# Optimization experiments

Measured on AMD Instinct MI355X. Metric: run time of the kernel, lower is better.

The kernel has to match this reference:

```python
import jax, jax.numpy as jnp
import numpy as np

B, C, L = 32, 512, 16          # batch, clauses per CNF, max literals per clause
D, H, P = 256, 1024, 16        # clause_hidden_dim, hidden_size, prefix_tokens
NH, NL = 8, 4                  # adapter_heads, adapter_layers
MAXV = 512                     # max_variables


def _ln(x, w, b, eps=1e-5):
    m = jnp.mean(x, axis=-1, keepdims=True)
    v = jnp.mean(jnp.square(x - m), axis=-1, keepdims=True)
    return (x - m) * jax.lax.rsqrt(v + eps) * w + b


def _mha(q, k, v, w_in, b_in, w_out, b_out, nh):
    E = q.shape[-1]
    dh = E // nh
    wq, wk, wv = jnp.split(w_in, 3, axis=0)
    bq, bk, bv = jnp.split(b_in, 3, axis=0)

    def heads(x, w, b):
        y = x @ w.T + b
        return y.reshape(x.shape[0], x.shape[1], nh, dh).transpose(0, 2, 1, 3)

    qh, kh, vh = heads(q, wq, bq), heads(k, wk, bk), heads(v, wv, bv)
    att = jax.nn.softmax(jnp.einsum('bhqd,bhkd->bhqk', qh, kh) * (1.0 / np.sqrt(dh)), axis=-1)
    o = jnp.einsum('bhqk,bhkd->bhqd', att, vh).transpose(0, 2, 1, 3).reshape(q.shape[0], q.shape[1], E)
    return o @ w_out.T + b_out


def setup_inputs() -> dict:
    key = jax.random.key(0)
    ks = jax.random.split(key, 16)
    s = 0.02
    var_idx = jax.random.randint(ks[0], (B, C, L), 0, MAXV + 1)
    sign_idx = jax.random.randint(ks[1], (B, C, L), 1, 3)   # 1=positive literal, 2=negative
    lens = jax.random.randint(ks[2], (B, C), 1, L + 1)      # ragged clause lengths >= 1
    lit_mask = jnp.arange(L)[None, None, :] < lens[..., None]
    inp = dict(var_idx=var_idx, sign_idx=sign_idx, lit_mask=lit_mask)
    inp['var_emb'] = jax.random.normal(ks[3], (MAXV + 1, D)) * s
    inp['sign_emb'] = jax.random.normal(ks[4], (3, D)) * s
    inp['litpos_emb'] = jax.random.normal(ks[5], (L, D)) * s
    inp['clausepos_emb'] = jax.random.normal(ks[6], (C, D)) * s
    inp['enc_in_w'] = jax.random.normal(ks[7], (NL, 3 * D, D)) * s
    inp['enc_in_b'] = jnp.zeros((NL, 3 * D))
    inp['enc_out_w'] = jax.random.normal(ks[8], (NL, D, D)) * s
    inp['enc_out_b'] = jnp.zeros((NL, D))
    inp['enc_ff1_w'] = jax.random.normal(ks[9], (NL, 4 * D, D)) * s
    inp['enc_ff1_b'] = jnp.zeros((NL, 4 * D))
    inp['enc_ff2_w'] = jax.random.normal(ks[10], (NL, D, 4 * D)) * s
    inp['enc_ff2_b'] = jnp.zeros((NL, D))
    inp['enc_n1_w'] = jnp.ones((NL, D))
    inp['enc_n1_b'] = jnp.zeros((NL, D))
    inp['enc_n2_w'] = jnp.ones((NL, D))
    inp['enc_n2_b'] = jnp.zeros((NL, D))
    inp['th_ln_w'] = jnp.ones((D,))
    inp['th_ln_b'] = jnp.zeros((D,))
    inp['th_w'] = jax.random.normal(ks[11], (H, D)) * s
    inp['th_b'] = jnp.zeros((H,))
    inp['pq'] = jax.random.normal(ks[12], (P, H))
    inp['pa_in_w'] = jax.random.normal(ks[13], (3 * H, H)) * s
    inp['pa_in_b'] = jnp.zeros((3 * H,))
    inp['pa_out_w'] = jax.random.normal(ks[14], (H, H)) * s
    inp['pa_out_b'] = jnp.zeros((H,))
    inp['pn_w'] = jnp.ones((H,))
    inp['pn_b'] = jnp.zeros((H,))
    return inp


def reference(var_idx, sign_idx, lit_mask, var_emb, sign_emb, litpos_emb, clausepos_emb,
              enc_in_w, enc_in_b, enc_out_w, enc_out_b, enc_ff1_w, enc_ff1_b,
              enc_ff2_w, enc_ff2_b, enc_n1_w, enc_n1_b, enc_n2_w, enc_n2_b,
              th_ln_w, th_ln_b, th_w, th_b, pq, pa_in_w, pa_in_b, pa_out_w, pa_out_b,
              pn_w, pn_b):
    # literal states [B,C,L,D]: four embedding gathers fused into one expression
    lit = (var_emb[var_idx] + sign_emb[sign_idx]
           + litpos_emb[None, None, :, :] + clausepos_emb[None, :, None, :])
    m = lit_mask[..., None].astype(lit.dtype)
    x = jnp.sum(lit * m, axis=2) / jnp.sum(m, axis=2)   # masked mean-pool -> [B,C,D]
    for i in range(NL):  # PyTorch post-norm TransformerEncoderLayer, gelu (exact)
        a = _mha(x, x, x, enc_in_w[i], enc_in_b[i], enc_out_w[i], enc_out_b[i], NH)
        x = _ln(x + a, enc_n1_w[i], enc_n1_b[i])
        f = jax.nn.gelu(x @ enc_ff1_w[i].T + enc_ff1_b[i], approximate=False) @ enc_ff2_w[i].T + enc_ff2_b[i]
        x = _ln(x + f, enc_n2_w[i], enc_n2_b[i])
    ch = _ln(x, th_ln_w, th_ln_b) @ th_w.T + th_b       # to_hidden -> [B,C,H]
    q = jnp.broadcast_to(pq[None], (ch.shape[0], P, H))
    pref = _mha(q, ch, ch, pa_in_w, pa_in_b, pa_out_w, pa_out_b, NH)
    return _ln(pref + q, pn_w, pn_b)                    # [B,P,H]
```

## Files before the change

kernel.cpp:

```cpp
#include <hip/hip_runtime.h>
#include <hip/hip_bf16.h>

typedef unsigned short u16;
typedef unsigned int u32;
typedef __attribute__((ext_vector_type(8))) short short8;
typedef __attribute__((ext_vector_type(4))) float floatx4;

#define BB 32
#define CC 512
#define LL 16
#define DD 256
#define HH 1024
#define PP 16
#define NLAY 4

__device__ __forceinline__ float bf2f(u16 u) {
  u32 x = ((u32)u) << 16; float f; __builtin_memcpy(&f, &x, 4); return f;
}
__device__ __forceinline__ u16 f2bf(float f) {
  __hip_bfloat16 h = __float2bfloat16(f);
  u16 r; __builtin_memcpy(&r, &h, 2); return r;
}
__device__ __forceinline__ void gload_lds16(const u16* g, u16* l) {
  __builtin_amdgcn_global_load_lds(
      (const __attribute__((address_space(1))) void*)g,
      (__attribute__((address_space(3))) void*)l, 16, 0, 0);
}

__global__ __launch_bounds__(256) void cvt_kernel(
    const float* __restrict__ s0, const float* __restrict__ s1,
    const float* __restrict__ s2, const float* __restrict__ s3,
    const float* __restrict__ s4, const float* __restrict__ s5,
    const float* __restrict__ s6, const float* __restrict__ s7,
    const float* __restrict__ s8, const float* __restrict__ s9,
    const float* __restrict__ s10, const float* __restrict__ s11,
    u16* __restrict__ dst)
{
  const float* srcs[12] = {s0, s1, s2, s3, s4, s5, s6, s7, s8, s9, s10, s11};
  const int pfx[12] = {786432, 1048576, 2097152, 3145728, 3407872, 6553600, 7602176,
                       7618560, 7749888, 7750656, 7754752, 7885824};
  int e = (blockIdx.x * 256 + threadIdx.x) * 4;
  int seg = 0;
  while (e >= pfx[seg]) seg++;
  int start = seg ? pfx[seg - 1] : 0;
  float4 f = *(const float4*)(srcs[seg] + (e - start));
  u16 o[4] = {f2bf(f.x), f2bf(f.y), f2bf(f.z), f2bf(f.w)};
  *(uint2*)(dst + e) = *(const uint2*)o;
}

__global__ __launch_bounds__(256) void thwT_kernel(
    const float* __restrict__ thw, u16* __restrict__ out)
{
  __shared__ float tile[32][33];
  int bx = blockIdx.x & 7, by = blockIdx.x >> 3;
  int tx = threadIdx.x & 31, ty = threadIdx.x >> 5;
  #pragma unroll
  for (int i = 0; i < 4; ++i) {
    int h = by * 32 + ty + i * 8, d = bx * 32 + tx;
    tile[ty + i * 8][tx] = thw[h * 256 + d];
  }
  __syncthreads();
  #pragma unroll
  for (int i = 0; i < 4; ++i) {
    int d = bx * 32 + ty + i * 8, h = by * 32 + tx;
    out[d * 1024 + h] = f2bf(tile[tx][ty + i * 8]);
  }
}

__global__ __launch_bounds__(256) void bT_kernel(
    const u16* __restrict__ in, u16* __restrict__ out)
{
  __shared__ u16 tile[32][33];
  int bx = blockIdx.x & 7, by = blockIdx.x >> 3;
  int tx = threadIdx.x & 31, ty = threadIdx.x >> 5;
  #pragma unroll
  for (int i = 0; i < 4; ++i) {
    int hd = by * 32 + ty + i * 8, c = bx * 32 + tx;
    tile[ty + i * 8][tx] = in[hd * 256 + c];
  }
  __syncthreads();
  #pragma unroll
  for (int i = 0; i < 4; ++i) {
    int c = bx * 32 + ty + i * 8, hd = by * 32 + tx;
    out[c * 1024 + hd] = tile[tx][ty + i * 8];
  }
}

__global__ __launch_bounds__(256) void qc_kernel(
    const u16* __restrict__ qh, const u16* __restrict__ wckT, u16* __restrict__ qcg)
{
  int h = blockIdx.x;
  int t = threadIdx.x, lane = t & 63, w = t >> 6;
  int mrow = lane & 15, quad = lane >> 4;
  const floatx4 zf = (floatx4){0.f, 0.f, 0.f, 0.f};
  floatx4 acc[4] = {zf, zf, zf, zf};
  #pragma unroll
  for (int kk = 0; kk < 4; ++kk) {
    short8 af = *(const short8*)(qh + (size_t)mrow * 1024 + h * 128 + kk * 32 + quad * 8);
    #pragma unroll
    for (int ct = 0; ct < 4; ++ct) {
      int c = w * 64 + ct * 16 + mrow;
      short8 bf = *(const short8*)(wckT + (size_t)c * 1024 + h * 128 + kk * 32 + quad * 8);
      acc[ct] = __builtin_amdgcn_mfma_f32_16x16x32_bf16(af, bf, acc[ct], 0, 0, 0);
    }
  }
  #pragma unroll
  for (int ct = 0; ct < 4; ++ct)
    #pragma unroll
    for (int r = 0; r < 4; ++r)
      qcg[((size_t)h * 16 + quad * 4 + r) * 256 + w * 64 + ct * 16 + mrow] = f2bf(acc[ct][r]);
}

__global__ __launch_bounds__(256) void biasfold_kernel(
    const u16* __restrict__ Wkv, const float* __restrict__ thb,
    const float* __restrict__ paib, float* __restrict__ out)
{
  int wv = threadIdx.x >> 6, lane = threadIdx.x & 63;
  int n = blockIdx.x * 4 + wv;
  const u16* wr = Wkv + (size_t)n * 1024;
  float s = 0.f;
  #pragma unroll
  for (int i = 0; i < 16; ++i) {
    int h = i * 64 + lane;
    s += bf2f(wr[h]) * thb[h];
  }
  #pragma unroll
  for (int off = 32; off; off >>= 1) s += __shfl_xor(s, off);
  if (!lane) out[n] = s + paib[1024 + n];
}

__global__ __launch_bounds__(256) void redk_kernel(
    const float* __restrict__ part, const float* __restrict__ bias,
    const float* __restrict__ res, float* __restrict__ outf, u16* __restrict__ outb,
    int N, int nz, int total, int flags)
{
  int idx = (blockIdx.x * 256 + threadIdx.x) * 4;
  if (idx >= total) return;
  float4 a = *(const float4*)(part + idx);
  for (int z = 1; z < nz; ++z) {
    float4 b = *(const float4*)(part + (size_t)z * total + idx);
    a.x += b.x; a.y += b.y; a.z += b.z; a.w += b.w;
  }
  int row = idx / N, col = idx - row * N;
  float v4[4] = {a.x, a.y, a.z, a.w};
  #pragma unroll
  for (int i = 0; i < 4; ++i) {
    if (bias) v4[i] += bias[col + i];
    if (res) v4[i] += res[(size_t)((flags & 4) ? (row & 15) : row) * N + col + i];
  }
  if (outf) {
    *(float4*)(outf + idx) = *(const float4*)v4;
  } else {
    u16 o[4] = {f2bf(v4[0]), f2bf(v4[1]), f2bf(v4[2]), f2bf(v4[3])};
    *(uint2*)(outb + idx) = *(const uint2*)o;
  }
}

__global__ __launch_bounds__(256) void embed_kernel(
    const int* __restrict__ vi, const int* __restrict__ si, const int* __restrict__ mk,
    const u16* __restrict__ veb, const u16* __restrict__ seb,
    const u16* __restrict__ lpeb, const u16* __restrict__ cpeb,
    u16* __restrict__ xb)
{
  int t = threadIdx.x;
  int bc = blockIdx.x * 2 + (t >> 7);
  int c = bc & (CC - 1);
  int dl = (t & 127) * 2;
  int base = bc * LL;
  float a0 = 0.f, a1 = 0.f; int cnt = 0;
  #pragma unroll
  for (int l = 0; l < LL; ++l) {
    if (mk[base + l]) {
      int v = vi[base + l], s = si[base + l];
      u32 vv = *(const u32*)&veb[v * DD + dl];
      u32 sv = *(const u32*)&seb[s * DD + dl];
      u32 lv = *(const u32*)&lpeb[l * DD + dl];
      a0 += bf2f((u16)vv) + bf2f((u16)sv) + bf2f((u16)lv);
      a1 += bf2f((u16)(vv >> 16)) + bf2f((u16)(sv >> 16)) + bf2f((u16)(lv >> 16));
      cnt++;
    }
  }
  u32 cv = *(const u32*)&cpeb[c * DD + dl];
  float inv = 1.f / (float)cnt;
  u32 pk = (u32)f2bf(a0 * inv + bf2f((u16)cv)) | ((u32)f2bf(a1 * inv + bf2f((u16)(cv >> 16))) << 16);
  *(u32*)&xb[(size_t)bc * DD + dl] = pk;
}

template<int NC, bool GELU, bool LN, bool DLN>
__global__ __launch_bounds__(256) void gwide_kernel(
    const u16* __restrict__ A, const u16* __restrict__ W, const float* __restrict__ bias,
    const u16* __restrict__ resb, const float* __restrict__ gam, const float* __restrict__ bet,
    const float* __restrict__ gam2, const float* __restrict__ bet2,
    u16* __restrict__ out, int N, int K)
{
  constexpr int NT = NC / 32;
  constexpr int NT4 = NC / 64;
  __shared__ __align__(16) u16 As[32 * 64];
  __shared__ __align__(16) u16 Ws[NC * 64];
  __shared__ float sred[32][4][2];
  __shared__ float sred2[32][4][2];
  int t = threadIdx.x, lane = t & 63, w = t >> 6;
  int mrow = lane & 15, quad = lane >> 4;
  int bn0 = blockIdx.x * NC, bm0 = blockIdx.y * 32;

  int rA = t >> 3, gcA = (t & 7) ^ (rA & 7);
  const u16* gAp = A + (size_t)(bm0 + rA) * K + gcA * 8;
  u16* lAp = As + (w * 64) * 8;
  const u16* gW0 = W + (size_t)(bn0 + rA) * K + gcA * 8;
  u16* lW0 = Ws + (w * 64) * 8;

  floatx4 acc[2][NT4];
  #pragma unroll
  for (int mi = 0; mi < 2; ++mi)
    #pragma unroll
    for (int nt = 0; nt < NT4; ++nt) acc[mi][nt] = (floatx4){0.f, 0.f, 0.f, 0.f};

  for (int k0 = 0; k0 < K; k0 += 64) {
    __syncthreads();
    gload_lds16(gAp, lAp); gAp += 64;
    #pragma unroll
    for (int i = 0; i < NT; ++i)
      gload_lds16(gW0 + (size_t)i * 32 * K, lW0 + i * 2048);
    gW0 += 64;
    __syncthreads();
    #pragma unroll
    for (int ks = 0; ks < 2; ++ks) {
      int sw = ((ks * 4 + quad) ^ (mrow & 7)) * 8;
      short8 af0 = *(const short8*)&As[mrow * 64 + sw];
      short8 af1 = *(const short8*)&As[(16 + mrow) * 64 + sw];
      #pragma unroll
      for (int nt = 0; nt < NT4; ++nt) {
        int rw = w * (NC / 4) + nt * 16 + mrow;
        short8 bf = *(const short8*)&Ws[rw * 64 + sw];
        acc[0][nt] = __builtin_amdgcn_mfma_f32_16x16x32_bf16(af0, bf, acc[0][nt], 0, 0, 0);
        acc[1][nt] = __builtin_amdgcn_mfma_f32_16x16x32_bf16(af1, bf, acc[1][nt], 0, 0, 0);
      }
    }
  }

  if constexpr (LN) {
    float val[2][NT4][4];
    float bv[NT4];
    #pragma unroll
    for (int nt = 0; nt < NT4; ++nt) bv[nt] = bias[w * 64 + nt * 16 + mrow];
    #pragma unroll
    for (int mi = 0; mi < 2; ++mi) {
      #pragma unroll
      for (int r = 0; r < 4; ++r) {
        int gm = bm0 + mi * 16 + quad * 4 + r;
        float sr = 0.f, s2r = 0.f;
        #pragma unroll
        for (int nt = 0; nt < NT4; ++nt) {
          int gn = w * 64 + nt * 16 + mrow;
          float v = acc[mi][nt][r] + bv[nt] + bf2f(resb[(size_t)gm * 256 + gn]);
          val[mi][nt][r] = v; sr += v; s2r += v * v;
        }
        sr += __shfl_xor(sr, 1); s2r += __shfl_xor(s2r, 1);
        sr += __shfl_xor(sr, 2); s2r += __shfl_xor(s2r, 2);
        sr += __shfl_xor(sr, 4); s2r += __shfl_xor(s2r, 4);
        sr += __shfl_xor(sr, 8); s2r += __shfl_xor(s2r, 8);
        if (mrow == 0) { sred[mi * 16 + quad * 4 + r][w][0] = sr; sred[mi * 16 + quad * 4 + r][w][1] = s2r; }
      }
    }
    __syncthreads();
    #pragma unroll
    for (int mi = 0; mi < 2; ++mi) {
      #pragma unroll
      for (int r = 0; r < 4; ++r) {
        int lrow = mi * 16 + quad * 4 + r;
        float S  = sred[lrow][0][0] + sred[lrow][1][0] + sred[lrow][2][0] + sred[lrow][3][0];
        float S2 = sred[lrow][0][1] + sred[lrow][1][1] + sred[lrow][2][1] + sred[lrow][3][1];
        float mean = S * (1.f / 256.f);
        float var = S2 * (1.f / 256.f) - mean * mean;
        float inv = rsqrtf(var + 1e-5f);
        float sr2 = 0.f, s2r2 = 0.f;
        #pragma unroll
        for (int nt = 0; nt < NT4; ++nt) {
          int gn = w * 64 + nt * 16 + mrow;
          float y = (val[mi][nt][r] - mean) * inv * gam[gn] + bet[gn];
          val[mi][nt][r] = y;
          if constexpr (DLN) { sr2 += y; s2r2 += y * y; }
          else out[(size_t)(bm0 + lrow) * 256 + gn] = f2bf(y);
        }
        if constexpr (DLN) {
          sr2 += __shfl_xor(sr2, 1); s2r2 += __shfl_xor(s2r2, 1);
          sr2 += __shfl_xor(sr2, 2); s2r2 += __shfl_xor(s2r2, 2);
          sr2 += __shfl_xor(sr2, 4); s2r2 += __shfl_xor(s2r2, 4);
          sr2 += __shfl_xor(sr2, 8); s2r2 += __shfl_xor(s2r2, 8);
          if (mrow == 0) { sred2[lrow][w][0] = sr2; sred2[lrow][w][1] = s2r2; }
        }
      }
    }
    if constexpr (DLN) {
      __syncthreads();
      #pragma unroll
      for (int mi = 0; mi < 2; ++mi) {
        #pragma unroll
        for (int r = 0; r < 4; ++r) {
          int lrow = mi * 16 + quad * 4 + r;
          float S  = sred2[lrow][0][0] + sred2[lrow][1][0] + sred2[lrow][2][0] + sred2[lrow][3][0];
          float S2 = sred2[lrow][0][1] + sred2[lrow][1][1] + sred2[lrow][2][1] + sred2[lrow][3][1];
          float mean = S * (1.f / 256.f);
          float var = S2 * (1.f / 256.f) - mean * mean;
          float inv = rsqrtf(var + 1e-5f);
          #pragma unroll
          for (int nt = 0; nt < NT4; ++nt) {
            int gn = w * 64 + nt * 16 + mrow;
            float z = (val[mi][nt][r] - mean) * inv * gam2[gn] + bet2[gn];
            out[(size_t)(bm0 + lrow) * 256 + gn] = f2bf(z);
          }
        }
      }
    }
  } else {
    #pragma unroll
    for (int nt = 0; nt < NT4; ++nt) {
      int gn = bn0 + w * (NC / 4) + nt * 16 + mrow;
      float bv = bias[gn];
      #pragma unroll
      for (int mi = 0; mi < 2; ++mi) {
        #pragma unroll
        for (int r = 0; r < 4; ++r) {
          int gm = bm0 + mi * 16 + quad * 4 + r;
          float v = acc[mi][nt][r] + bv;
          if (GELU) v = 0.5f * v * (1.f + erff(v * 0.70710678118654752f));
          out[(size_t)gm * N + gn] = f2bf(v);
        }
      }
    }
  }
}

__global__ __launch_bounds__(256) void gemm128_kernel(
    const u16* __restrict__ A, const u16* __restrict__ W, const float* __restrict__ bias,
    const float* __restrict__ res, void* __restrict__ out,
    int M, int N, int K, int flags)
{
  __shared__ __align__(16) u16 As[128 * 64];
  __shared__ __align__(16) u16 Bs[128 * 64];
  int t = threadIdx.x;
  int lane = t & 63, w = t >> 6;
  int wm = w & 1, wn = w >> 1;
  int bn0 = blockIdx.x * 128, bm0 = blockIdx.y * 128;
  int mrow = lane & 15, quad = lane >> 4;
  int z = blockIdx.z, NZ = gridDim.z;
  int Kc = K / NZ, kbase = z * Kc;

  const u16* gA[4]; const u16* gB[4];
  u16* lA[4]; u16* lB[4];
  #pragma unroll
  for (int it = 0; it < 4; ++it) {
    int c = w * 256 + it * 64 + lane;
    int r = c >> 3;
    int gc = (c & 7) ^ (r & 7);
    gA[it] = A + (size_t)(bm0 + r) * K + kbase + gc * 8;
    gB[it] = W + (size_t)(bn0 + r) * K + kbase + gc * 8;
    lA[it] = As + (w * 256 + it * 64) * 8;
    lB[it] = Bs + (w * 256 + it * 64) * 8;
  }
  floatx4 acc[4][4];
  #pragma unroll
  for (int i = 0; i < 4; ++i)
    #pragma unroll
    for (int j = 0; j < 4; ++j)
      acc[i][j] = (floatx4){0.f, 0.f, 0.f, 0.f};
  int sw0 = ((0 * 4 + quad) ^ (mrow & 7)) * 8;
  int sw1 = ((1 * 4 + quad) ^ (mrow & 7)) * 8;

  for (int k0 = 0; k0 < Kc; k0 += 64) {
    __syncthreads();
    #pragma unroll
    for (int it = 0; it < 4; ++it) { gload_lds16(gA[it], lA[it]); gA[it] += 64; }
    #pragma unroll
    for (int it = 0; it < 4; ++it) { gload_lds16(gB[it], lB[it]); gB[it] += 64; }
    __syncthreads();
    #pragma unroll
    for (int ks = 0; ks < 2; ++ks) {
      int sw = ks ? sw1 : sw0;
      short8 af[4], bfr[4];
      #pragma unroll
      for (int mi = 0; mi < 4; ++mi)
        af[mi] = *(const short8*)&As[(wm * 64 + mi * 16 + mrow) * 64 + sw];
      #pragma unroll
      for (int nj = 0; nj < 4; ++nj)
        bfr[nj] = *(const short8*)&Bs[(wn * 64 + nj * 16 + mrow) * 64 + sw];
      #pragma unroll
      for (int mi = 0; mi < 4; ++mi)
        #pragma unroll
        for (int nj = 0; nj < 4; ++nj)
          acc[mi][nj] = __builtin_amdgcn_mfma_f32_16x16x32_bf16(af[mi], bfr[nj], acc[mi][nj], 0, 0, 0);
    }
  }
  if (NZ > 1) {
    float* po = (float*)out + (size_t)z * M * N;
    #pragma unroll
    for (int nj = 0; nj < 4; ++nj) {
      int gn = bn0 + wn * 64 + nj * 16 + mrow;
      #pragma unroll
      for (int mi = 0; mi < 4; ++mi)
        #pragma unroll
        for (int r = 0; r < 4; ++r) {
          int gm = bm0 + wm * 64 + mi * 16 + quad * 4 + r;
          po[(size_t)gm * N + gn] = acc[mi][nj][r];
        }
    }
    return;
  }
  bool do_gelu = (flags & 1) != 0, of32 = (flags & 2) != 0;
  #pragma unroll
  for (int nj = 0; nj < 4; ++nj) {
    int gn = bn0 + wn * 64 + nj * 16 + mrow;
    float bv = bias ? bias[gn] : 0.f;
    #pragma unroll
    for (int mi = 0; mi < 4; ++mi) {
      #pragma unroll
      for (int r = 0; r < 4; ++r) {
        int gm = bm0 + wm * 64 + mi * 16 + quad * 4 + r;
        float v = acc[mi][nj][r] + bv;
        if (do_gelu) v = 0.5f * v * (1.f + erff(v * 0.70710678118654752f));
        if (flags & 4) v += res[(size_t)(gm & 15) * N + gn];
        else if (res) v += res[(size_t)gm * N + gn];
        if (of32) ((float*)out)[(size_t)gm * N + gn] = v;
        else      ((u16*)out)[(size_t)gm * N + gn] = f2bf(v);
      }
    }
  }
}

template<int D>
__global__ __launch_bounds__(256) void lnw_kernel(
    const float* __restrict__ in, const float* __restrict__ w, const float* __restrict__ b,
    float* __restrict__ outf, u16* __restrict__ outb)
{
  constexpr int NV = D / 64;
  int lane = threadIdx.x & 63, wv = threadIdx.x >> 6;
  int row = blockIdx.x * 4 + wv;
  const float* xr = in + (size_t)row * D;
  float v[NV];
  float s = 0.f, s2 = 0.f;
  #pragma unroll
  for (int i = 0; i < NV; ++i) {
    v[i] = xr[lane + i * 64];
    s += v[i]; s2 += v[i] * v[i];
  }
  #pragma unroll
  for (int off = 32; off > 0; off >>= 1) { s += __shfl_xor(s, off); s2 += __shfl_xor(s2, off); }
  float mean = s / (float)D;
  float var = s2 / (float)D - mean * mean;
  float inv = rsqrtf(var + 1e-5f);
  #pragma unroll
  for (int i = 0; i < NV; ++i) {
    int col = lane + i * 64;
    float y = (v[i] - mean) * inv * w[col] + b[col];
    size_t o = (size_t)row * D + col;
    if (outf) outf[o] = y;
    if (outb) outb[o] = f2bf(y);
  }
}

__global__ __launch_bounds__(256, 5) void attn_enc6_kernel(
    const u16* __restrict__ qkv, u16* __restrict__ out)
{
  __shared__ __align__(16) u16 Ks[64 * 40];
  __shared__ __align__(16) u16 Vt[32 * 72];
  __shared__ __align__(16) u16 Pl[4 * 32 * 72];
  int F = blockIdx.x;
  int xcd = F & 7, jj = F >> 3;
  int pair = xcd * 32 + (jj >> 2), qt = jj & 3;
  int b = pair >> 3, h = pair & 7;
  int t = threadIdx.x, lane = t & 63, w = t >> 6;
  int mrow = lane & 15, quad = lane >> 4;
  int q0 = qt * 128 + w * 32;
  short8 qf[2];
  #pragma unroll
  for (int mi = 0; mi < 2; ++mi)
    qf[mi] = *(const short8*)(qkv + (size_t)(b * CC + q0 + mi * 16 + mrow) * 768 + h * 32 + quad * 8);
  floatx4 o[2][2];
  #pragma unroll
  for (int mi = 0; mi < 2; ++mi)
    #pragma unroll
    for (int di = 0; di < 2; ++di) o[mi][di] = (floatx4){0.f, 0.f, 0.f, 0.f};
  float lst[2][4] = {{0.f,0.f,0.f,0.f},{0.f,0.f,0.f,0.f}};
  const float sc = 0.17677669529663687f * 1.4426950408889634f;
  const floatx4 zf = (floatx4){0.f, 0.f, 0.f, 0.f};
  for (int jt = 0; jt < 8; ++jt) {
    if (jt) __syncthreads();
    {
      int j = t >> 2, q4 = (t & 3) * 8;
      uint4 kk = *(const uint4*)(qkv + (size_t)(b * CC + jt * 64 + j) * 768 + 256 + h * 32 + q4);
      *(uint4*)&Ks[j * 40 + q4] = kk;
      uint4 vv = *(const uint4*)(qkv + (size_t)(b * CC + jt * 64 + j) * 768 + 512 + h * 32 + q4);
      u16 tmp[8]; *(uint4*)tmp = vv;
      int jp = (j & 15) * 4 + (j >> 4);
      #pragma unroll
      for (int i = 0; i < 8; ++i) Vt[(q4 + i) * 72 + jp] = tmp[i];
    }
    __syncthreads();
    floatx4 s[2][4];
    #pragma unroll
    for (int nj = 0; nj < 4; ++nj) {
      short8 bf = *(const short8*)&Ks[(nj * 16 + mrow) * 40 + quad * 8];
      s[0][nj] = __builtin_amdgcn_mfma_f32_16x16x32_bf16(qf[0], bf, zf, 0, 0, 0);
      s[1][nj] = __builtin_amdgcn_mfma_f32_16x16x32_bf16(qf[1], bf, zf, 0, 0, 0);
    }
    #pragma unroll
    for (int mi = 0; mi < 2; ++mi) {
      #pragma unroll
      for (int r = 0; r < 4; ++r) {
        float ps = 0.f; u16 hv[4];
        #pragma unroll
        for (int nj = 0; nj < 4; ++nj) {
          float p = exp2f(s[mi][nj][r] * sc);
          ps += p; hv[nj] = f2bf(p);
        }
        lst[mi][r] += ps;
        *(uint2*)&Pl[(w * 32 + mi * 16 + quad * 4 + r) * 72 + mrow * 4] = *(uint2*)hv;
      }
    }
    #pragma unroll
    for (int ks = 0; ks < 2; ++ks) {
      short8 a0 = *(const short8*)&Pl[(w * 32 + mrow) * 72 + ks * 32 + quad * 8];
      short8 a1 = *(const short8*)&Pl[(w * 32 + 16 + mrow) * 72 + ks * 32 + quad * 8];
      short8 b0 = *(const short8*)&Vt[mrow * 72 + ks * 32 + quad * 8];
      short8 b1 = *(const short8*)&Vt[(16 + mrow) * 72 + ks * 32 + quad * 8];
      o[0][0] = __builtin_amdgcn_mfma_f32_16x16x32_bf16(a0, b0, o[0][0], 0, 0, 0);
      o[0][1] = __builtin_amdgcn_mfma_f32_16x16x32_bf16(a0, b1, o[0][1], 0, 0, 0);
      o[1][0] = __builtin_amdgcn_mfma_f32_16x16x32_bf16(a1, b0, o[1][0], 0, 0, 0);
      o[1][1] = __builtin_amdgcn_mfma_f32_16x16x32_bf16(a1, b1, o[1][1], 0, 0, 0);
    }
  }
  #pragma unroll
  for (int mi = 0; mi < 2; ++mi) {
    #pragma unroll
    for (int r = 0; r < 4; ++r) {
      float l = lst[mi][r];
      l += __shfl_xor(l, 1); l += __shfl_xor(l, 2);
      l += __shfl_xor(l, 4); l += __shfl_xor(l, 8);
      float inv = 1.f / l;
      int row = b * CC + q0 + mi * 16 + quad * 4 + r;
      #pragma unroll
      for (int di = 0; di < 2; ++di)
        out[(size_t)row * DD + h * 32 + di * 16 + mrow] = f2bf(o[mi][di][r] * inv);
    }
  }
}

__global__ __launch_bounds__(256) void attn_preff_kernel(
    const u16* __restrict__ tln, const u16* __restrict__ wcb,
    const u16* __restrict__ qcg, const float* __restrict__ bkv,
    u16* __restrict__ out)
{
  __shared__ __align__(16) u16 Ajc[64 * 264];
  __shared__ __align__(16) u16 Acj[256 * 72];
  __shared__ __align__(16) u16 Qs[16 * 264];
  __shared__ __align__(16) u16 Ps[16 * 72];
  __shared__ __align__(16) u16 Ts[16 * 264];
  __shared__ float Lred[4][16];
  int b = blockIdx.x, h = blockIdx.y;
  int t = threadIdx.x, lane = t & 63, w = t >> 6;
  int mrow = lane & 15, quad = lane >> 4;
  const float sc = 0.08838834764831845f * 1.4426950408889634f;
  const floatx4 zf = (floatx4){0.f, 0.f, 0.f, 0.f};
  {
    int q = t >> 4, c0 = (t & 15) * 16;
    *(uint4*)&Qs[q * 264 + c0]     = *(const uint4*)(qcg + ((size_t)h * 16 + q) * 256 + c0);
    *(uint4*)&Qs[q * 264 + c0 + 8] = *(const uint4*)(qcg + ((size_t)h * 16 + q) * 256 + c0 + 8);
  }
  floatx4 Tacc[4] = {zf, zf, zf, zf};
  float lacc = 0.f;
  const u16* tb = tln + (size_t)b * 512 * 256;
  for (int jt = 0; jt < 8; ++jt) {
    __syncthreads();
    {
      int j = t >> 2, c0 = (t & 3) * 64;
      #pragma unroll
      for (int u = 0; u < 8; ++u) {
        uint4 v = *(const uint4*)(tb + (size_t)(jt * 64 + j) * 256 + c0 + u * 8);
        *(uint4*)&Ajc[j * 264 + c0 + u * 8] = v;
        u16 tmp[8]; *(uint4*)tmp = v;
        #pragma unroll
        for (int i = 0; i < 8; ++i) Acj[(c0 + u * 8 + i) * 72 + j] = tmp[i];
      }
    }
    __syncthreads();
    floatx4 s = zf;
    #pragma unroll
    for (int kk = 0; kk < 8; ++kk) {
      short8 af = *(const short8*)&Ajc[(w * 16 + mrow) * 264 + kk * 32 + quad * 8];
      short8 bf = *(const short8*)&Qs[mrow * 264 + kk * 32 + quad * 8];
      s = __builtin_amdgcn_mfma_f32_16x16x32_bf16(af, bf, s, 0, 0, 0);
    }
    u16 hv[4]; float ps = 0.f;
    #pragma unroll
    for (int r = 0; r < 4; ++r) {
      float p = exp2f(s[r] * sc);
      ps += p; hv[r] = f2bf(p);
    }
    ps += __shfl_xor(ps, 16); ps += __shfl_xor(ps, 32);
    lacc += ps;
    *(uint2*)&Ps[mrow * 72 + w * 16 + quad * 4] = *(uint2*)hv;
    __syncthreads();
    #pragma unroll
    for (int kk = 0; kk < 2; ++kk) {
      short8 af = *(const short8*)&Ps[mrow * 72 + kk * 32 + quad * 8];
      #pragma unroll
      for (int ct = 0; ct < 4; ++ct) {
        short8 bf = *(const short8*)&Acj[(w * 64 + ct * 16 + mrow) * 72 + kk * 32 + quad * 8];
        Tacc[ct] = __builtin_amdgcn_mfma_f32_16x16x32_bf16(af, bf, Tacc[ct], 0, 0, 0);
      }
    }
  }
  if (lane < 16) Lred[w][lane] = lacc;
  __syncthreads();
  #pragma unroll
  for (int r = 0; r < 4; ++r) {
    int q = quad * 4 + r;
    float l = Lred[0][q] + Lred[1][q] + Lred[2][q] + Lred[3][q];
    float inv = 1.f / l;
    #pragma unroll
    for (int ct = 0; ct < 4; ++ct)
      Ts[q * 264 + w * 64 + ct * 16 + mrow] = f2bf(Tacc[ct][r] * inv);
  }
  __syncthreads();
  const u16* wv = wcb + (size_t)(1024 + h * 128) * 256;
  floatx4 oacc[2] = {zf, zf};
  #pragma unroll
  for (int kk = 0; kk < 8; ++kk) {
    short8 af = *(const short8*)&Ts[mrow * 264 + kk * 32 + quad * 8];
    #pragma unroll
    for (int dt = 0; dt < 2; ++dt) {
      short8 bf = *(const short8*)(wv + (size_t)(w * 32 + dt * 16 + mrow) * 256 + kk * 32 + quad * 8);
      oacc[dt] = __builtin_amdgcn_mfma_f32_16x16x32_bf16(af, bf, oacc[dt], 0, 0, 0);
    }
  }
  #pragma unroll
  for (int dt = 0; dt < 2; ++dt) {
    int d = w * 32 + dt * 16 + mrow;
    float bv = bkv[1024 + h * 128 + d];
    #pragma unroll
    for (int r = 0; r < 4; ++r) {
      int q = quad * 4 + r;
      out[((size_t)(b * 16 + q)) * 1024 + h * 128 + d] = f2bf(oacc[dt][r] + bv);
    }
  }
}

extern "C" void kernel_launch(void* const* d_in, const int* in_sizes, int n_in,
                              void* d_out, int out_size, void* d_ws, size_t ws_size,
                              hipStream_t stream)
{
  const int* vi = (const int*)d_in[0];
  const int* si = (const int*)d_in[1];
  const int* mk = (const int*)d_in[2];
  const float* ve   = (const float*)d_in[3];
  const float* se   = (const float*)d_in[4];
  const float* lpe  = (const float*)d_in[5];
  const float* cpe  = (const float*)d_in[6];
  const float* eiw  = (const float*)d_in[7];
  const float* eib  = (const float*)d_in[8];
  const float* eow  = (const float*)d_in[9];
  const float* eob  = (const float*)d_in[10];
  const float* f1w  = (const float*)d_in[11];
  const float* f1b  = (const float*)d_in[12];
  const float* f2w  = (const float*)d_in[13];
  const float* f2b  = (const float*)d_in[14];
  const float* n1w  = (const float*)d_in[15];
  const float* n1b  = (const float*)d_in[16];
  const float* n2w  = (const float*)d_in[17];
  const float* n2b  = (const float*)d_in[18];
  const float* tlw  = (const float*)d_in[19];
  const float* tlb  = (const float*)d_in[20];
  const float* thw  = (const float*)d_in[21];
  const float* thb  = (const float*)d_in[22];
  const float* pq   = (const float*)d_in[23];
  const float* paiw = (const float*)d_in[24];
  const float* paib = (const float*)d_in[25];
  const float* paow = (const float*)d_in[26];
  const float* paob = (const float*)d_in[27];
  const float* pnw  = (const float*)d_in[28];
  const float* pnb  = (const float*)d_in[29];

  const int NROW = BB * CC;
  const size_t MB = 1048576;
  char* base = (char*)d_ws;
  u16* xb   = (u16*)(base);
  u16* qkvb = (u16*)(base + 8 * MB);
  u16* atto = (u16*)(base + 32 * MB);
  u16* h1   = (u16*)(base + 8 * MB);
  u16* tln  = (u16*)(base + 96 * MB);
  u16* wcb   = (u16*)(base + 64 * MB);
  u16* thwTb = (u16*)(base + 65 * MB);
  float* bkv = (float*)(base + 66 * MB);
  u16* wckT  = (u16*)(base + 67 * MB);
  u16* qcg   = (u16*)(base + 68 * MB);
  float* skpart = (float*)(base + 80 * MB);
  u16* wbf  = (u16*)(base + 104 * MB);
  u16* qh    = (u16*)(base + 120 * MB);
  u16* prefo = (u16*)(base + 121 * MB);
  float* prefout = (float*)(base + 122 * MB);

  u16* eiw_b  = wbf + 0;
  u16* eow_b  = wbf + 786432;
  u16* f1w_b  = wbf + 1048576;
  u16* f2w_b  = wbf + 2097152;
  u16* thw_b  = wbf + 3145728;
  u16* paiw_b = wbf + 3407872;
  u16* paow_b = wbf + 6553600;
  u16* pqb    = wbf + 7602176;
  u16* veb    = wbf + 7618560;
  u16* seb    = wbf + 7749888;
  u16* lpeb   = wbf + 7750656;
  u16* cpeb   = wbf + 7754752;

  dim3 blk(256);
  cvt_kernel<<<7701, blk, 0, stream>>>(eiw, eow, f1w, f2w, thw, paiw, paow, pq,
                                       ve, se, lpe, cpe, wbf);
  thwT_kernel<<<256, blk, 0, stream>>>(thw, thwTb);
  biasfold_kernel<<<512, blk, 0, stream>>>(paiw_b + (size_t)HH * HH, thb, paib, bkv);
  gemm128_kernel<<<dim3(2, 16, 4), blk, 0, stream>>>(
      paiw_b + (size_t)HH * HH, thwTb, nullptr, nullptr, skpart, 2048, 256, HH, 0);
  redk_kernel<<<512, blk, 0, stream>>>(skpart, nullptr, nullptr, nullptr, wcb,
                                       256, 4, 2048 * 256, 0);
  gemm128_kernel<<<dim3(8, 1, 8), blk, 0, stream>>>(
      pqb, paiw_b, nullptr, nullptr, skpart, 128, 1024, HH, 0);
  redk_kernel<<<128, blk, 0, stream>>>(skpart, paib, nullptr, nullptr, qh,
                                       1024, 8, 128 * 1024, 0);
  bT_kernel<<<256, blk, 0, stream>>>(wcb, wckT);
  qc_kernel<<<8, blk, 0, stream>>>(qh, wckT, qcg);
  embed_kernel<<<NROW/2, blk, 0, stream>>>(vi, si, mk, veb, seb, lpeb, cpeb, xb);
  for (int i = 0; i < NLAY; ++i) {
    gwide_kernel<384, false, false, false><<<dim3(2, NROW/32), blk, 0, stream>>>(
        xb, eiw_b + (size_t)i*768*DD, eib + i*768, nullptr, nullptr, nullptr, nullptr, nullptr,
        qkvb, 768, DD);
    attn_enc6_kernel<<<1024, blk, 0, stream>>>(qkvb, atto);
    gwide_kernel<256, false, true, false><<<dim3(1, NROW/32), blk, 0, stream>>>(
        atto, eow_b + (size_t)i*DD*DD, eob + i*DD, xb, n1w + i*DD, n1b + i*DD, nullptr, nullptr,
        xb, DD, DD);
    gwide_kernel<256, true, false, false><<<dim3(4, NROW/32), blk, 0, stream>>>(
        xb, f1w_b + (size_t)i*HH*DD, f1b + i*HH, nullptr, nullptr, nullptr, nullptr, nullptr,
        h1, HH, DD);
    if (i < NLAY - 1) {
      gwide_kernel<256, false, true, false><<<dim3(1, NROW/32), blk, 0, stream>>>(
          h1, f2w_b + (size_t)i*DD*HH, f2b + i*DD, xb, n2w + i*DD, n2b + i*DD, nullptr, nullptr,
          xb, DD, HH);
    } else {
      gwide_kernel<256, false, true, true><<<dim3(1, NROW/32), blk, 0, stream>>>(
          h1, f2w_b + (size_t)i*DD*HH, f2b + i*DD, xb, n2w + i*DD, n2b + i*DD, tlw, tlb,
          tln, DD, HH);
    }
  }
  attn_preff_kernel<<<dim3(BB, 8), blk, 0, stream>>>(tln, wcb, qcg, bkv, prefo);
  gemm128_kernel<<<dim3(1024/128, (BB*PP)/128, 4), blk, 0, stream>>>(
      prefo, paow_b, nullptr, nullptr, skpart, BB*PP, HH, HH, 0);
  redk_kernel<<<512, blk, 0, stream>>>(skpart, paob, pq, prefout, nullptr,
                                       1024, 4, BB*PP*HH, 4);
  lnw_kernel<1024><<<(BB*PP)/4, blk, 0, stream>>>(prefout, pnw, pnb, (float*)d_out, nullptr);
}
```

Before: 658.3 us.

## Fuse encoder FFN up-projection, GELU and down-projection into one kernel

Replaces the separate FF1 (with GELU) and FF2 (with residual and LayerNorm) GEMM launches with a single kernel. Each 32-row block computes 256-column chunks of the hidden activation into LDS and immediately accumulates them into the output, so the 16384x1024 bf16 intermediate never goes to global memory. In exchange, each block reloads the full FF1 and FF2 weights, the kernel has no double buffering, and the grid is only 512 blocks with a large LDS footprint, which may limit occupancy. Output and residual alias the same buffer, which is safe because each block reads its residual rows before writing them.

```diff
diff --git a/kernel.cpp b/kernel.cpp
--- a/kernel.cpp
+++ b/kernel.cpp
@@ -325,6 +325,179 @@
           float v = acc[mi][nt][r] + bv;
           if (GELU) v = 0.5f * v * (1.f + erff(v * 0.70710678118654752f));
           out[(size_t)gm * N + gn] = f2bf(v);
+        }
+      }
+    }
+  }
+}
+
+template<bool DLN>
+__global__ __launch_bounds__(256) void ffu_kernel(
+    const u16* __restrict__ A, const u16* __restrict__ W1, const float* __restrict__ b1,
+    const u16* __restrict__ W2, const float* __restrict__ b2,
+    const u16* __restrict__ resb,
+    const float* __restrict__ gam, const float* __restrict__ bet,
+    const float* __restrict__ gam2, const float* __restrict__ bet2,
+    u16* __restrict__ out)
+{
+  __shared__ __align__(16) u16 As[2048];
+  __shared__ __align__(16) u16 Ws[8 * 2048];
+  __shared__ __align__(16) u16 Hs[4 * 2048];
+  int t = threadIdx.x, lane = t & 63, w = t >> 6;
+  int mrow = lane & 15, quad = lane >> 4;
+  int bm0 = blockIdx.x * 32;
+  int rA = t >> 3, gcA = (t & 7) ^ (rA & 7);
+
+  floatx4 yacc[2][4];
+  #pragma unroll
+  for (int mi = 0; mi < 2; ++mi)
+    #pragma unroll
+    for (int nt = 0; nt < 4; ++nt) yacc[mi][nt] = (floatx4){0.f, 0.f, 0.f, 0.f};
+
+  for (int nq = 0; nq < 4; ++nq) {
+    floatx4 hacc[2][4];
+    #pragma unroll
+    for (int mi = 0; mi < 2; ++mi)
+      #pragma unroll
+      for (int nt = 0; nt < 4; ++nt) hacc[mi][nt] = (floatx4){0.f, 0.f, 0.f, 0.f};
+    for (int kt = 0; kt < 4; ++kt) {
+      __syncthreads();
+      gload_lds16(A + (size_t)(bm0 + rA) * 256 + kt * 64 + gcA * 8, As + (w * 64) * 8);
+      #pragma unroll
+      for (int i = 0; i < 8; ++i)
+        gload_lds16(W1 + (size_t)(nq * 256 + i * 32 + rA) * 256 + kt * 64 + gcA * 8,
+                    Ws + i * 2048 + (w * 64) * 8);
+      __syncthreads();
+      #pragma unroll
+      for (int ks = 0; ks < 2; ++ks) {
+        int sw = ((ks * 4 + quad) ^ (mrow & 7)) * 8;
+        short8 af0 = *(const short8*)&As[mrow * 64 + sw];
+        short8 af1 = *(const short8*)&As[(16 + mrow) * 64 + sw];
+        #pragma unroll
+        for (int nt = 0; nt < 4; ++nt) {
+          short8 bf = *(const short8*)&Ws[(w * 64 + nt * 16 + mrow) * 64 + sw];
+          hacc[0][nt] = __builtin_amdgcn_mfma_f32_16x16x32_bf16(af0, bf, hacc[0][nt], 0, 0, 0);
+          hacc[1][nt] = __builtin_amdgcn_mfma_f32_16x16x32_bf16(af1, bf, hacc[1][nt], 0, 0, 0);
+        }
+      }
+    }
+    {
+      float bv1[4];
+      #pragma unroll
+      for (int nt = 0; nt < 4; ++nt) bv1[nt] = b1[nq * 256 + w * 64 + nt * 16 + mrow];
+      #pragma unroll
+      for (int mi = 0; mi < 2; ++mi) {
+        #pragma unroll
+        for (int nt = 0; nt < 4; ++nt) {
+          int g = nt * 2 + (mrow >> 3);
+          #pragma unroll
+          for (int r = 0; r < 4; ++r) {
+            int row = mi * 16 + quad * 4 + r;
+            float v = hacc[mi][nt][r] + bv1[nt];
+            v = 0.5f * v * (1.f + erff(v * 0.70710678118654752f));
+            Hs[w * 2048 + row * 64 + (g ^ (row & 7)) * 8 + (mrow & 7)] = f2bf(v);
+          }
+        }
+      }
+    }
+    for (int kt2 = 0; kt2 < 4; ++kt2) {
+      __syncthreads();
+      #pragma unroll
+      for (int i = 0; i < 8; ++i)
+        gload_lds16(W2 + (size_t)(i * 32 + rA) * 1024 + nq * 256 + kt2 * 64 + gcA * 8,
+                    Ws + i * 2048 + (w * 64) * 8);
+      __syncthreads();
+      #pragma unroll
+      for (int ks = 0; ks < 2; ++ks) {
+        int sw = ((ks * 4 + quad) ^ (mrow & 7)) * 8;
+        short8 af0 = *(const short8*)&Hs[kt2 * 2048 + mrow * 64 + sw];
+        short8 af1 = *(const short8*)&Hs[kt2 * 2048 + (16 + mrow) * 64 + sw];
+        #pragma unroll
+        for (int nt = 0; nt < 4; ++nt) {
+          short8 bf = *(const short8*)&Ws[(w * 64 + nt * 16 + mrow) * 64 + sw];
+          yacc[0][nt] = __builtin_amdgcn_mfma_f32_16x16x32_bf16(af0, bf, yacc[0][nt], 0, 0, 0);
+          yacc[1][nt] = __builtin_amdgcn_mfma_f32_16x16x32_bf16(af1, bf, yacc[1][nt], 0, 0, 0);
+        }
+      }
+    }
+  }
+  __syncthreads();
+  float* sred  = (float*)Hs;
+  float* sred2 = (float*)(Hs + 2048);
+  float val[2][4][4];
+  float bv[4];
+  #pragma unroll
+  for (int nt = 0; nt < 4; ++nt) bv[nt] = b2[w * 64 + nt * 16 + mrow];
+  #pragma unroll
+  for (int mi = 0; mi < 2; ++mi) {
+    #pragma unroll
+    for (int r = 0; r < 4; ++r) {
+      int gm = bm0 + mi * 16 + quad * 4 + r;
+      float sr = 0.f, s2r = 0.f;
+      #pragma unroll
+      for (int nt = 0; nt < 4; ++nt) {
+        int gn = w * 64 + nt * 16 + mrow;
+        float v = yacc[mi][nt][r] + bv[nt] + bf2f(resb[(size_t)gm * 256 + gn]);
+        val[mi][nt][r] = v; sr += v; s2r += v * v;
+      }
+      sr += __shfl_xor(sr, 1); s2r += __shfl_xor(s2r, 1);
+      sr += __shfl_xor(sr, 2); s2r += __shfl_xor(s2r, 2);
+      sr += __shfl_xor(sr, 4); s2r += __shfl_xor(s2r, 4);
+      sr += __shfl_xor(sr, 8); s2r += __shfl_xor(s2r, 8);
+      if (mrow == 0) {
+        int lrow = mi * 16 + quad * 4 + r;
+        sred[lrow * 8 + w * 2 + 0] = sr; sred[lrow * 8 + w * 2 + 1] = s2r;
+      }
+    }
+  }
+  __syncthreads();
+  #pragma unroll
+  for (int mi = 0; mi < 2; ++mi) {
+    #pragma unroll
+    for (int r = 0; r < 4; ++r) {
+      int lrow = mi * 16 + quad * 4 + r;
+      float S  = sred[lrow * 8 + 0] + sred[lrow * 8 + 2] + sred[lrow * 8 + 4] + sred[lrow * 8 + 6];
+      float S2 = sred[lrow * 8 + 1] + sred[lrow * 8 + 3] + sred[lrow * 8 + 5] + sred[lrow * 8 + 7];
+      float mean = S * (1.f / 256.f);
+      float var = S2 * (1.f / 256.f) - mean * mean;
+      float inv = rsqrtf(var + 1e-5f);
+      float sr2 = 0.f, s2r2 = 0.f;
+      #pragma unroll
+      for (int nt = 0; nt < 4; ++nt) {
+        int gn = w * 64 + nt * 16 + mrow;
+        float y = (val[mi][nt][r] - mean) * inv * gam[gn] + bet[gn];
+        val[mi][nt][r] = y;
+        if constexpr (DLN) { sr2 += y; s2r2 += y * y; }
+        else out[(size_t)(bm0 + lrow) * 256 + gn] = f2bf(y);
+      }
+      if constexpr (DLN) {
+        sr2 += __shfl_xor(sr2, 1); s2r2 += __shfl_xor(s2r2, 1);
+        sr2 += __shfl_xor(sr2, 2); s2r2 += __shfl_xor(s2r2, 2);
+        sr2 += __shfl_xor(sr2, 4); s2r2 += __shfl_xor(s2r2, 4);
+        sr2 += __shfl_xor(sr2, 8); s2r2 += __shfl_xor(s2r2, 8);
+        if (mrow == 0) {
+          sred2[lrow * 8 + w * 2 + 0] = sr2; sred2[lrow * 8 + w * 2 + 1] = s2r2;
+        }
+      }
+    }
+  }
+  if constexpr (DLN) {
+    __syncthreads();
+    #pragma unroll
+    for (int mi = 0; mi < 2; ++mi) {
+      #pragma unroll
+      for (int r = 0; r < 4; ++r) {
+        int lrow = mi * 16 + quad * 4 + r;
+        float S  = sred2[lrow * 8 + 0] + sred2[lrow * 8 + 2] + sred2[lrow * 8 + 4] + sred2[lrow * 8 + 6];
+        float S2 = sred2[lrow * 8 + 1] + sred2[lrow * 8 + 3] + sred2[lrow * 8 + 5] + sred2[lrow * 8 + 7];
+        float mean = S * (1.f / 256.f);
+        float var = S2 * (1.f / 256.f) - mean * mean;
+        float inv = rsqrtf(var + 1e-5f);
+        #pragma unroll
+        for (int nt = 0; nt < 4; ++nt) {
+          int gn = w * 64 + nt * 16 + mrow;
+          float z = (val[mi][nt][r] - mean) * inv * gam2[gn] + bet2[gn];
+          out[(size_t)(bm0 + lrow) * 256 + gn] = f2bf(z);
         }
       }
     }
@@ -686,7 +859,6 @@
   u16* xb   = (u16*)(base);
   u16* qkvb = (u16*)(base + 8 * MB);
   u16* atto = (u16*)(base + 32 * MB);
-  u16* h1   = (u16*)(base + 8 * MB);
   u16* tln  = (u16*)(base + 96 * MB);
   u16* wcb   = (u16*)(base + 64 * MB);
   u16* thwTb = (u16*)(base + 65 * MB);
@@ -736,17 +908,14 @@
     gwide_kernel<256, false, true, false><<<dim3(1, NROW/32), blk, 0, stream>>>(
         atto, eow_b + (size_t)i*DD*DD, eob + i*DD, xb, n1w + i*DD, n1b + i*DD, nullptr, nullptr,
         xb, DD, DD);
-    gwide_kernel<256, true, false, false><<<dim3(4, NROW/32), blk, 0, stream>>>(
-        xb, f1w_b + (size_t)i*HH*DD, f1b + i*HH, nullptr, nullptr, nullptr, nullptr, nullptr,
-        h1, HH, DD);
     if (i < NLAY - 1) {
-      gwide_kernel<256, false, true, false><<<dim3(1, NROW/32), blk, 0, stream>>>(
-          h1, f2w_b + (size_t)i*DD*HH, f2b + i*DD, xb, n2w + i*DD, n2b + i*DD, nullptr, nullptr,
-          xb, DD, HH);
+      ffu_kernel<false><<<NROW/32, blk, 0, stream>>>(
+          xb, f1w_b + (size_t)i*HH*DD, f1b + i*HH, f2w_b + (size_t)i*DD*HH, f2b + i*DD,
+          xb, n2w + i*DD, n2b + i*DD, nullptr, nullptr, xb);
     } else {
-      gwide_kernel<256, false, true, true><<<dim3(1, NROW/32), blk, 0, stream>>>(
-          h1, f2w_b + (size_t)i*DD*HH, f2b + i*DD, xb, n2w + i*DD, n2b + i*DD, tlw, tlb,
-          tln, DD, HH);
+      ffu_kernel<true><<<NROW/32, blk, 0, stream>>>(
+          xb, f1w_b + (size_t)i*HH*DD, f1b + i*HH, f2w_b + (size_t)i*DD*HH, f2b + i*DD,
+          xb, n2w + i*DD, n2b + i*DD, tlw, tlb, tln);
     }
   }
   attn_preff_kernel<<<dim3(BB, 8), blk, 0, stream>>>(tln, wcb, qcg, bkv, prefo);
```

Result: no change. 659.1 us (median of 3 runs) (+0.1%).
